# Kernel tuning notes

Measured on AMD Instinct MI355X. Metric: run time of the kernel, lower is better.

## Reference

```python
import jax, jax.numpy as jnp
import numpy as np

LN_EPS = 1e-5
NORM_EPS = 1e-12  # torch F.normalize default eps


def _layernorm(x, gamma, beta):
    mu = x.mean(axis=-1, keepdims=True)
    var = ((x - mu) ** 2).mean(axis=-1, keepdims=True)
    return (x - mu) * jax.lax.rsqrt(var + LN_EPS) * gamma + beta


def _l2norm(x, axis):
    n = jnp.sqrt((x ** 2).sum(axis=axis, keepdims=True))
    return x / jnp.maximum(n, NORM_EPS)


def setup_inputs() -> dict:
    key = jax.random.key(0)
    ks = jax.random.split(key, 4)
    B, N, D, E, S, H = 64, 256, 1024, 16, 16, 256
    x = jax.random.normal(ks[0], (B, N, D), dtype=jnp.float32)
    mu = jax.random.normal(ks[1], (D, E, S), dtype=jnp.float32) / np.sqrt(D)
    w1 = jax.random.normal(ks[2], (E, D, H), dtype=jnp.float32) * np.sqrt(2.0 / D)
    w2 = jax.random.normal(ks[3], (E, H, D), dtype=jnp.float32) * np.sqrt(2.0 / (H + D))
    return {
        'x': x,
        'ln_gamma': jnp.ones((D,), jnp.float32),
        'ln_beta': jnp.zeros((D,), jnp.float32),
        'mu': mu,
        'scale': jnp.ones((1,), jnp.float32),
        'w1': w1,
        'b1': jnp.zeros((E, H), jnp.float32),
        'w2': w2,
        'b2': jnp.zeros((E, D), jnp.float32),
    }


def reference(x, ln_gamma, ln_beta, mu, scale, w1, b1, w2, b2):
    B, N, D = x.shape
    _, E, S = mu.shape
    # LayerNorm then cosine-similarity logits (eval mode: no noise, no dropout)
    xn = _layernorm(x, ln_gamma, ln_beta)                      # [B,N,D]
    x_unit = _l2norm(xn, axis=-1)                              # [B,N,D]
    mu_unit = _l2norm(mu, axis=0)                              # [D,E,S]
    logits = jnp.einsum('bnd,des->bnes', x_unit * scale, mu_unit)  # [B,N,E,S]
    # dispatch: softmax over tokens n; combine: softmax over flattened slots (e,s)
    dispatch = jax.nn.softmax(logits, axis=1)                  # [B,N,E,S]
    combine = jax.nn.softmax(logits.reshape(B, N, E * S), axis=-1).reshape(B, N, E, S)
    # dispatch tokens to slots
    slot_in = jnp.einsum('bnd,bnes->besd', xn, dispatch)       # [B,E,S,D]
    # batched per-expert MLP (GELU exact, matches nn.GELU default)
    h = jax.nn.gelu(jnp.einsum('besd,edh->besh', slot_in, w1) + b1[None, :, None, :], approximate=False)
    slot_out = jnp.einsum('besh,ehd->besd', h, w2) + b2[None, :, None, :]
    # combine slots back to tokens
    out = jnp.einsum('besd,bnes->bnd', slot_out, combine)      # [B,N,D]
    return out
```

## Files before the change

### kernel.cpp

```cpp
#include <hip/hip_runtime.h>

#define DD 1024
#define NN 256
#define BB 64
#define EE 16
#define SS 16
#define HH 256
#define ES 256
#define BN 16384

typedef unsigned short u16;
typedef unsigned int u32;
typedef __attribute__((ext_vector_type(8))) short bf16x8;
typedef __attribute__((ext_vector_type(4))) float f32x4;

#define MFMA(a, b, c) __builtin_amdgcn_mfma_f32_16x16x32_bf16(a, b, c, 0, 0, 0)

__device__ __forceinline__ u16 f2b(float f) {
  union { float f; u32 i; } c; c.f = f;
  u32 i = c.i;
  u32 r = (i + 0x7FFFu + ((i >> 16) & 1u)) >> 16;
  return (u16)r;
}

__device__ __forceinline__ float bredsum(float v, float* red) {
  #pragma unroll
  for (int o = 32; o > 0; o >>= 1) v += __shfl_down(v, o, 64);
  __syncthreads();
  if ((threadIdx.x & 63) == 0) red[threadIdx.x >> 6] = v;
  __syncthreads();
  return red[0] + red[1] + red[2] + red[3];
}

__global__ __launch_bounds__(256) void k_stats(
    const float* __restrict__ x, const float* __restrict__ gamma,
    const float* __restrict__ beta, const float* __restrict__ scale,
    float* __restrict__ mean_, float* __restrict__ rstd_,
    float* __restrict__ fct_) {
  __shared__ float red[4];
  int bn = blockIdx.x, t = threadIdx.x;
  float4 u = ((const float4*)(x + (size_t)bn * DD))[t];
  float s = u.x + u.y + u.z + u.w;
  float ss = u.x * u.x + u.y * u.y + u.z * u.z + u.w * u.w;
  s = bredsum(s, red);
  ss = bredsum(ss, red);
  float mean = s * (1.0f / DD);
  float var = ss * (1.0f / DD) - mean * mean;
  float rstd = rsqrtf(var + 1e-5f);
  float4 g = ((const float4*)gamma)[t];
  float4 be = ((const float4*)beta)[t];
  float x0 = (u.x - mean) * rstd * g.x + be.x;
  float x1 = (u.y - mean) * rstd * g.y + be.y;
  float x2 = (u.z - mean) * rstd * g.z + be.z;
  float x3 = (u.w - mean) * rstd * g.w + be.w;
  float s2 = x0 * x0 + x1 * x1 + x2 * x2 + x3 * x3;
  s2 = bredsum(s2, red);
  float f = scale[0] / fmaxf(sqrtf(s2), 1e-12f);
  if (t == 0) { mean_[bn] = mean; rstd_[bn] = rstd; fct_[bn] = f; }
}

__global__ __launch_bounds__(256) void k_rmun(
    const float* __restrict__ mu, const float* __restrict__ gamma,
    const float* __restrict__ beta, float* __restrict__ rmun,
    float* __restrict__ c3, float* __restrict__ c4) {
  __shared__ float red[4];
  int es = blockIdx.x, t = threadIdx.x;
  float ss = 0.f, s3 = 0.f, s4 = 0.f;
  #pragma unroll
  for (int j = 0; j < 4; j++) {
    int d = t + j * 256;
    float v = mu[(size_t)d * ES + es];
    ss += v * v;
    s3 += gamma[d] * v;
    s4 += beta[d] * v;
  }
  ss = bredsum(ss, red);
  s3 = bredsum(s3, red);
  s4 = bredsum(s4, red);
  if (t == 0) {
    float r = 1.0f / fmaxf(sqrtf(ss), 1e-12f);
    rmun[es] = r;
    c3[es] = s3 * r;
    c4[es] = s4 * r;
  }
}

__global__ __launch_bounds__(256) void k_mut(
    const float* __restrict__ mu, const float* __restrict__ gamma,
    const float* __restrict__ rmun, u16* __restrict__ muT) {
  __shared__ u16 L[256 * 70];
  int t = threadIdx.x;
  int d0 = blockIdx.x * 64;
  float rm = rmun[t];
  for (int i = 0; i < 64; i++) {
    int d = d0 + i;
    float gv = gamma[d];
    L[t * 70 + i] = f2b(mu[(size_t)d * ES + t] * rm * gv);
  }
  __syncthreads();
  u32 buf[32];
  #pragma unroll
  for (int k2 = 0; k2 < 32; k2++)
    buf[k2] = *(const u32*)&L[t * 70 + k2 * 2];
  u16* dst = muT + (size_t)t * DD + d0;
  #pragma unroll
  for (int k4 = 0; k4 < 8; k4++) {
    uint4 o;
    o.x = buf[k4 * 4]; o.y = buf[k4 * 4 + 1];
    o.z = buf[k4 * 4 + 2]; o.w = buf[k4 * 4 + 3];
    *(uint4*)(dst + k4 * 8) = o;
  }
}

__global__ __launch_bounds__(256) void k_xt(
    const float* __restrict__ x, u16* __restrict__ xT) {
  __shared__ u16 L[256 * 70];
  int t = threadIdx.x;
  int bn0 = blockIdx.x * 64;
  for (int cch = 0; cch < 4; cch++) {
    __syncthreads();
    for (int r = 0; r < 64; r++)
      L[t * 70 + r] = f2b(x[(size_t)(bn0 + r) * DD + cch * 256 + t]);
    __syncthreads();
    u32 buf[32];
    #pragma unroll
    for (int k2 = 0; k2 < 32; k2++)
      buf[k2] = *(const u32*)&L[t * 70 + k2 * 2];
    u16* dst = xT + (size_t)(cch * 256 + t) * BN + bn0;
    #pragma unroll
    for (int k4 = 0; k4 < 8; k4++) {
      uint4 o;
      o.x = buf[k4 * 4]; o.y = buf[k4 * 4 + 1];
      o.z = buf[k4 * 4 + 2]; o.w = buf[k4 * 4 + 3];
      *(uint4*)(dst + k4 * 8) = o;
    }
  }
}

__global__ __launch_bounds__(256) void k_tr(
    const float* __restrict__ src, u16* __restrict__ dst, int R, int C) {
  __shared__ u16 T[64 * 70];
  int t = threadIdx.x;
  int e = blockIdx.y;
  int tR = R >> 6;
  int r0 = (blockIdx.x % tR) * 64;
  int c0 = (blockIdx.x / tR) * 64;
  #pragma unroll
  for (int i = 0; i < 16; i++) {
    int r = r0 + i * 4 + (t >> 6);
    int c = t & 63;
    T[c * 70 + i * 4 + (t >> 6)] = f2b(src[((size_t)e * R + r) * C + c0 + c]);
  }
  __syncthreads();
  int cl = t >> 2, rsg = (t & 3) * 16;
  u32 buf[8];
  #pragma unroll
  for (int k2 = 0; k2 < 8; k2++)
    buf[k2] = *(const u32*)&T[cl * 70 + rsg + k2 * 2];
  u16* dp = dst + ((size_t)e * C + c0 + cl) * R + r0 + rsg;
  uint4 o0, o1;
  o0.x = buf[0]; o0.y = buf[1]; o0.z = buf[2]; o0.w = buf[3];
  o1.x = buf[4]; o1.y = buf[5]; o1.z = buf[6]; o1.w = buf[7];
  *(uint4*)dp = o0;
  *(uint4*)(dp + 8) = o1;
}

__global__ __launch_bounds__(256) void k_logits_mfma(
    const float* __restrict__ x, const u16* __restrict__ muT,
    const float* __restrict__ mean_, const float* __restrict__ rstd_,
    const float* __restrict__ fct_, const float* __restrict__ c3,
    const float* __restrict__ c4, float* __restrict__ logitsT) {
  __shared__ u16 xb[64 * 136];
  int t = threadIdx.x;
  int lane = t & 63, w = t >> 6, q = lane >> 4, m16 = lane & 15;
  int bn0 = blockIdx.x * 64;
  int es0 = w * 64;
  f32x4 z = {0.f, 0.f, 0.f, 0.f};
  f32x4 acc[4][4];
  #pragma unroll
  for (int mt = 0; mt < 4; mt++)
    #pragma unroll
    for (int nt = 0; nt < 4; nt++) acc[mt][nt] = z;
  int sr = t >> 5, cc = (t & 31) * 4;
  for (int kb = 0; kb < 8; kb++) {
    __syncthreads();
    #pragma unroll
    for (int it = 0; it < 8; it++) {
      int row = sr + it * 8;
      float4 v = *(const float4*)(x + (size_t)(bn0 + row) * DD + kb * 128 + cc);
      uint2 pk;
      pk.x = (u32)f2b(v.x) | ((u32)f2b(v.y) << 16);
      pk.y = (u32)f2b(v.z) | ((u32)f2b(v.w) << 16);
      *(uint2*)&xb[row * 136 + cc] = pk;
    }
    __syncthreads();
    #pragma unroll
    for (int ks = 0; ks < 4; ks++) {
      int k = ks * 32 + q * 8;
      bf16x8 a[4];
      #pragma unroll
      for (int mt = 0; mt < 4; mt++)
        a[mt] = *(const bf16x8*)(muT + (size_t)(es0 + mt * 16 + m16) * DD +
                                 kb * 128 + k);
      #pragma unroll
      for (int nt = 0; nt < 4; nt++) {
        bf16x8 bb = *(const bf16x8*)&xb[(nt * 16 + m16) * 136 + k];
        #pragma unroll
        for (int mt = 0; mt < 4; mt++)
          acc[mt][nt] = MFMA(a[mt], bb, acc[mt][nt]);
      }
    }
  }
  #pragma unroll
  for (int nt = 0; nt < 4; nt++) {
    int bn = bn0 + nt * 16 + m16;
    float fv = fct_[bn], rv = rstd_[bn], mv = mean_[bn];
    #pragma unroll
    for (int mt = 0; mt < 4; mt++)
      #pragma unroll
      for (int i = 0; i < 4; i++) {
        int es = es0 + mt * 16 + q * 4 + i;
        float val = fv * (rv * acc[mt][nt][i] - rv * mv * c3[es] + c4[es]);
        logitsT[(size_t)es * BN + bn] = val;
      }
  }
}

__global__ __launch_bounds__(256) void k_disp(
    const float* __restrict__ logitsT, const float* __restrict__ mean_,
    const float* __restrict__ rstd_, u16* __restrict__ dispW,
    float* __restrict__ c1g) {
  int t = threadIdx.x;
  int e = blockIdx.x, b = blockIdx.y;
  int s = t >> 4, c = t & 15;
  const float* lrow = logitsT + (size_t)(e * 16 + s) * BN + b * 256 + c * 16;
  float lv[16];
  #pragma unroll
  for (int i2 = 0; i2 < 4; i2++) {
    float4 f = *(const float4*)(lrow + i2 * 4);
    lv[i2 * 4 + 0] = f.x; lv[i2 * 4 + 1] = f.y;
    lv[i2 * 4 + 2] = f.z; lv[i2 * 4 + 3] = f.w;
  }
  float mx = -1e30f;
  #pragma unroll
  for (int i = 0; i < 16; i++) mx = fmaxf(mx, lv[i]);
  #pragma unroll
  for (int o = 1; o < 16; o <<= 1) mx = fmaxf(mx, __shfl_xor(mx, o, 64));
  float sum = 0.f;
  #pragma unroll
  for (int i = 0; i < 16; i++) { lv[i] = __expf(lv[i] - mx); sum += lv[i]; }
  #pragma unroll
  for (int o = 1; o < 16; o <<= 1) sum += __shfl_xor(sum, o, 64);
  float inv = 1.0f / sum;
  float c1p = 0.f;
  u16 wp[16];
  #pragma unroll
  for (int i = 0; i < 16; i++) {
    int n = c * 16 + i;
    float wv = lv[i] * inv * rstd_[b * 256 + n];
    c1p += wv * mean_[b * 256 + n];
    wp[i] = f2b(wv);
  }
  #pragma unroll
  for (int o = 1; o < 16; o <<= 1) c1p += __shfl_xor(c1p, o, 64);
  if (c == 0) c1g[(b << 8) + e * 16 + s] = c1p;
  u16* drow = dispW + ((size_t)(b * 256 + e * 16 + s)) * 256 + c * 16;
  #pragma unroll
  for (int i2 = 0; i2 < 4; i2++) {
    uint2 pk;
    pk.x = (u32)wp[i2 * 4] | ((u32)wp[i2 * 4 + 1] << 16);
    pk.y = (u32)wp[i2 * 4 + 2] | ((u32)wp[i2 * 4 + 3] << 16);
    *(uint2*)(drow + i2 * 4) = pk;
  }
}

__global__ __launch_bounds__(256) void k_slotin(
    const u16* __restrict__ xT, const u16* __restrict__ dispW,
    const float* __restrict__ c1g, const float* __restrict__ gamma,
    const float* __restrict__ beta, u16* __restrict__ SI) {
  __shared__ u16 xb[128 * 264];
  int t = threadIdx.x;
  int lane = t & 63, w = t >> 6, q = lane >> 4, m16 = lane & 15;
  int d0 = blockIdx.x * 128, b = blockIdx.y;
  #pragma unroll
  for (int it = 0; it < 16; it++) {
    int c = it * 256 + t;
    int row = c >> 5, off = (c & 31) * 8;
    uint4 v = *(const uint4*)(xT + (size_t)(d0 + row) * BN + b * 256 + off);
    *(uint4*)&xb[row * 264 + off] = v;
  }
  __syncthreads();
  f32x4 z = {0.f, 0.f, 0.f, 0.f};
  f32x4 acc[4][8];
  #pragma unroll
  for (int mt = 0; mt < 4; mt++)
    #pragma unroll
    for (int nt = 0; nt < 8; nt++) acc[mt][nt] = z;
  int es0 = w * 64;
  for (int ks = 0; ks < 8; ks++) {
    int k = ks * 32 + q * 8;
    bf16x8 a[4];
    #pragma unroll
    for (int mt = 0; mt < 4; mt++)
      a[mt] = *(const bf16x8*)(dispW +
               ((size_t)(b * 256 + es0 + mt * 16 + m16)) * 256 + k);
    #pragma unroll
    for (int nt = 0; nt < 8; nt++) {
      bf16x8 bb = *(const bf16x8*)&xb[(nt * 16 + m16) * 264 + k];
      #pragma unroll
      for (int mt = 0; mt < 4; mt++) acc[mt][nt] = MFMA(a[mt], bb, acc[mt][nt]);
    }
  }
  float gv[8], bev[8];
  #pragma unroll
  for (int nt = 0; nt < 8; nt++) {
    int d = d0 + nt * 16 + m16;
    gv[nt] = gamma[d]; bev[nt] = beta[d];
  }
  #pragma unroll
  for (int mt = 0; mt < 4; mt++) {
    float c1[4];
    #pragma unroll
    for (int i = 0; i < 4; i++)
      c1[i] = c1g[(b << 8) + es0 + mt * 16 + q * 4 + i];
    #pragma unroll
    for (int nt = 0; nt < 8; nt++)
      #pragma unroll
      for (int i = 0; i < 4; i++)
        SI[((size_t)(w * 4 + mt) * 1024 + b * 16 + q * 4 + i) * DD + d0 +
           nt * 16 + m16] = f2b(gv[nt] * (acc[mt][nt][i] - c1[i]) + bev[nt]);
  }
}

__global__ __launch_bounds__(256) void k_mlp1(
    const u16* __restrict__ SI, const u16* __restrict__ w1T,
    const float* __restrict__ b1, u16* __restrict__ H) {
  __shared__ u16 At[64 * 72];
  __shared__ u16 Bt[64 * 72];
  int t = threadIdx.x;
  int lane = t & 63, w = t >> 6, q = lane >> 4, m16 = lane & 15;
  int nt0 = blockIdx.x * 64;
  int mt0 = blockIdx.y * 64;
  int e = blockIdx.z;
  int wm = (w & 1) * 32, wn = (w >> 1) * 32;
  f32x4 z = {0.f, 0.f, 0.f, 0.f};
  f32x4 acc[2][2];
  #pragma unroll
  for (int mt = 0; mt < 2; mt++)
    #pragma unroll
    for (int nt = 0; nt < 2; nt++) acc[mt][nt] = z;
  const u16* Ab = SI + ((size_t)e * 1024 + mt0) * DD;
  const u16* Bb = w1T + ((size_t)e * HH + nt0) * DD;
  int row = t >> 2, off = (t & 3) * 16;
  uint4 pa0, pa1, pb0, pb1;
  pa0 = *(const uint4*)(Ab + (size_t)row * DD + off);
  pa1 = *(const uint4*)(Ab + (size_t)row * DD + off + 8);
  pb0 = *(const uint4*)(Bb + (size_t)row * DD + off);
  pb1 = *(const uint4*)(Bb + (size_t)row * DD + off + 8);
  for (int kb = 0; kb < 16; kb++) {
    *(uint4*)&At[row * 72 + off] = pa0;
    *(uint4*)&At[row * 72 + off + 8] = pa1;
    *(uint4*)&Bt[row * 72 + off] = pb0;
    *(uint4*)&Bt[row * 72 + off + 8] = pb1;
    __syncthreads();
    if (kb < 15) {
      int k0 = (kb + 1) * 64;
      pa0 = *(const uint4*)(Ab + (size_t)row * DD + k0 + off);
      pa1 = *(const uint4*)(Ab + (size_t)row * DD + k0 + off + 8);
      pb0 = *(const uint4*)(Bb + (size_t)row * DD + k0 + off);
      pb1 = *(const uint4*)(Bb + (size_t)row * DD + k0 + off + 8);
    }
    #pragma unroll
    for (int kk = 0; kk < 2; kk++) {
      int k = kk * 32 + q * 8;
      bf16x8 a[2], bb[2];
      #pragma unroll
      for (int mt = 0; mt < 2; mt++)
        a[mt] = *(const bf16x8*)&At[(wm + mt * 16 + m16) * 72 + k];
      #pragma unroll
      for (int nt = 0; nt < 2; nt++)
        bb[nt] = *(const bf16x8*)&Bt[(wn + nt * 16 + m16) * 72 + k];
      #pragma unroll
      for (int mt = 0; mt < 2; mt++)
        #pragma unroll
        for (int nt = 0; nt < 2; nt++)
          acc[mt][nt] = MFMA(a[mt], bb[nt], acc[mt][nt]);
    }
    __syncthreads();
  }
  #pragma unroll
  for (int nt = 0; nt < 2; nt++) {
    int h = nt0 + wn + nt * 16 + m16;
    float b1v = b1[e * HH + h];
    #pragma unroll
    for (int mt = 0; mt < 2; mt++)
      #pragma unroll
      for (int i = 0; i < 4; i++) {
        float zz = acc[mt][nt][i] + b1v;
        int bs = mt0 + wm + mt * 16 + q * 4 + i;
        H[((size_t)e * 1024 + bs) * HH + h] =
            f2b(0.5f * zz * (1.0f + erff(zz * 0.70710678118654752f)));
      }
  }
}

__global__ __launch_bounds__(256) void k_mlp2(
    const u16* __restrict__ H, const u16* __restrict__ w2T,
    const float* __restrict__ b2, u16* __restrict__ SO) {
  __shared__ u16 At[128 * 72];
  __shared__ u16 Bt[128 * 72];
  int t = threadIdx.x;
  int lane = t & 63, w = t >> 6, q = lane >> 4, m16 = lane & 15;
  int nt0 = blockIdx.x * 128;
  int mt0 = blockIdx.y * 128;
  int e = blockIdx.z;
  int wm = (w & 1) * 64, wn = (w >> 1) * 64;
  f32x4 z = {0.f, 0.f, 0.f, 0.f};
  f32x4 acc[4][4];
  #pragma unroll
  for (int mt = 0; mt < 4; mt++)
    #pragma unroll
    for (int nt = 0; nt < 4; nt++) acc[mt][nt] = z;
  const u16* Ab = H + ((size_t)e * 1024 + mt0) * HH;
  const u16* Bb = w2T + ((size_t)e * DD + nt0) * HH;
  for (int kb = 0; kb < 4; kb++) {
    __syncthreads();
    #pragma unroll
    for (int it = 0; it < 4; it++) {
      int c = it * 256 + t;
      int row = c >> 3, off = (c & 7) * 8;
      *(uint4*)&At[row * 72 + off] =
          *(const uint4*)(Ab + (size_t)row * HH + kb * 64 + off);
      *(uint4*)&Bt[row * 72 + off] =
          *(const uint4*)(Bb + (size_t)row * HH + kb * 64 + off);
    }
    __syncthreads();
    #pragma unroll
    for (int kk = 0; kk < 2; kk++) {
      int k = kk * 32 + q * 8;
      bf16x8 a[4], bb[4];
      #pragma unroll
      for (int mt = 0; mt < 4; mt++)
        a[mt] = *(const bf16x8*)&At[(wm + mt * 16 + m16) * 72 + k];
      #pragma unroll
      for (int nt = 0; nt < 4; nt++)
        bb[nt] = *(const bf16x8*)&Bt[(wn + nt * 16 + m16) * 72 + k];
      #pragma unroll
      for (int mt = 0; mt < 4; mt++)
        #pragma unroll
        for (int nt = 0; nt < 4; nt++)
          acc[mt][nt] = MFMA(a[mt], bb[nt], acc[mt][nt]);
    }
  }
  #pragma unroll
  for (int nt = 0; nt < 4; nt++) {
    int d = nt0 + wn + nt * 16 + m16;
    float b2v = b2[e * DD + d];
    #pragma unroll
    for (int mt = 0; mt < 4; mt++)
      #pragma unroll
      for (int i = 0; i < 4; i++) {
        int bs = mt0 + wm + mt * 16 + q * 4 + i;
        SO[((size_t)e * 1024 + bs) * DD + d] = f2b(acc[mt][nt][i] + b2v);
      }
  }
}

__global__ __launch_bounds__(256) void k_out_mfma(
    const u16* __restrict__ slot_out, const float* __restrict__ logitsT,
    float* __restrict__ out) {
  __shared__ u16 comb[32 * 264];
  __shared__ u16 sot[64 * 264];
  __shared__ float red[8][32];
  int t = threadIdx.x;
  int lane = t & 63, w = t >> 6, q = lane >> 4, m16 = lane & 15;
  int id = blockIdx.x;
  int b = (id & 7) * 8 + ((id >> 3) & 7);
  int dc = id >> 6;
  {
    int es2 = (t & 127) * 2, dh = t >> 7;
    const u16* s0 = slot_out +
        ((size_t)((es2 >> 4) * 1024 + b * 16 + (es2 & 15))) * DD +
        dc * 64 + dh * 32;
    const u16* s1 = s0 + DD;
    #pragma unroll
    for (int k2 = 0; k2 < 8; k2++) {
      ushort4 r0 = *(const ushort4*)(s0 + k2 * 4);
      ushort4 r1 = *(const ushort4*)(s1 + k2 * 4);
      int dl = dh * 32 + k2 * 4;
      *(u32*)&sot[(dl + 0) * 264 + es2] = (u32)r0.x | ((u32)r1.x << 16);
      *(u32*)&sot[(dl + 1) * 264 + es2] = (u32)r0.y | ((u32)r1.y << 16);
      *(u32*)&sot[(dl + 2) * 264 + es2] = (u32)r0.z | ((u32)r1.z << 16);
      *(u32*)&sot[(dl + 3) * 264 + es2] = (u32)r0.w | ((u32)r1.w << 16);
    }
  }
  for (int nch = 0; nch < 8; nch++) {
    int n0 = nch * 32;
    __syncthreads();
    {
      int j = t & 31, ch = t >> 5;
      float lv[32];
      const float* base = logitsT + (size_t)(ch * 32) * BN + b * 256 + n0 + j;
      #pragma unroll
      for (int i = 0; i < 32; i++) lv[i] = base[(size_t)i * BN];
      float mx = -1e30f;
      #pragma unroll
      for (int i = 0; i < 32; i++) mx = fmaxf(mx, lv[i]);
      red[ch][j] = mx;
      __syncthreads();
      mx = red[0][j];
      #pragma unroll
      for (int k = 1; k < 8; k++) mx = fmaxf(mx, red[k][j]);
      __syncthreads();
      float sum = 0.f;
      #pragma unroll
      for (int i = 0; i < 32; i++) { lv[i] = __expf(lv[i] - mx); sum += lv[i]; }
      red[ch][j] = sum;
      __syncthreads();
      sum = 0.f;
      #pragma unroll
      for (int k = 0; k < 8; k++) sum += red[k][j];
      float inv = 1.0f / sum;
      #pragma unroll
      for (int i2 = 0; i2 < 8; i2++) {
        uint2 pk;
        pk.x = (u32)f2b(lv[i2 * 4] * inv) | ((u32)f2b(lv[i2 * 4 + 1] * inv) << 16);
        pk.y = (u32)f2b(lv[i2 * 4 + 2] * inv) | ((u32)f2b(lv[i2 * 4 + 3] * inv) << 16);
        *(uint2*)&comb[j * 264 + ch * 32 + i2 * 4] = pk;
      }
    }
    __syncthreads();
    f32x4 aA = {0.f, 0.f, 0.f, 0.f}, aB = {0.f, 0.f, 0.f, 0.f};
    #pragma unroll
    for (int ks = 0; ks < 8; ks++) {
      bf16x8 bb = *(const bf16x8*)&sot[(w * 16 + m16) * 264 + ks * 32 + q * 8];
      bf16x8 a0 = *(const bf16x8*)&comb[m16 * 264 + ks * 32 + q * 8];
      bf16x8 a1 = *(const bf16x8*)&comb[(16 + m16) * 264 + ks * 32 + q * 8];
      aA = MFMA(a0, bb, aA);
      aB = MFMA(a1, bb, aB);
    }
    int d = dc * 64 + w * 16 + m16;
    #pragma unroll
    for (int i = 0; i < 4; i++) {
      out[((size_t)b * NN + n0 + q * 4 + i) * DD + d] = aA[i];
      out[((size_t)b * NN + n0 + 16 + q * 4 + i) * DD + d] = aB[i];
    }
  }
}

extern "C" void kernel_launch(void* const* d_in, const int* in_sizes, int n_in,
                              void* d_out, int out_size, void* d_ws, size_t ws_size,
                              hipStream_t stream) {
  const float* x     = (const float*)d_in[0];
  const float* gamma = (const float*)d_in[1];
  const float* beta  = (const float*)d_in[2];
  const float* mu    = (const float*)d_in[3];
  const float* scale = (const float*)d_in[4];
  const float* w1    = (const float*)d_in[5];
  const float* b1    = (const float*)d_in[6];
  const float* w2    = (const float*)d_in[7];
  const float* b2    = (const float*)d_in[8];
  float* out = (float*)d_out;

  const size_t WS_NEED = 50531328;
  if (ws_size < WS_NEED) return;
  char* ws = (char*)d_ws;
  u16*   sislot  = (u16*)(ws);
  float* logitsT = (float*)(ws + 33554432);
  float* mean_   = (float*)(ws + 50331648);
  float* rstd_   = (float*)(ws + 50397184);
  float* fct_    = (float*)(ws + 50462720);
  float* rmun    = (float*)(ws + 50528256);
  float* c3      = (float*)(ws + 50529280);
  float* c4      = (float*)(ws + 50530304);

  char* sc = (char*)d_out;
  u16* xT    = (u16*)(sc);
  u16* w1T   = (u16*)(sc + 33554432);
  u16* w2T   = (u16*)(sc + 41943040);
  u16* dispW = (u16*)(sc + 50331648);
  u16* muT   = (u16*)(sc + 58720256);
  float* c1g = (float*)(sc + 59244544);
  u16* Hbuf  = (u16*)(sc + 58720256);

  k_stats<<<BN, 256, 0, stream>>>(x, gamma, beta, scale, mean_, rstd_, fct_);
  k_rmun<<<ES, 256, 0, stream>>>(mu, gamma, beta, rmun, c3, c4);
  k_mut<<<16, 256, 0, stream>>>(mu, gamma, rmun, muT);
  k_xt<<<BN / 64, 256, 0, stream>>>(x, xT);
  k_tr<<<dim3(64, EE), 256, 0, stream>>>(w1, w1T, DD, HH);
  k_tr<<<dim3(64, EE), 256, 0, stream>>>(w2, w2T, HH, DD);
  k_logits_mfma<<<BN / 64, 256, 0, stream>>>(x, muT, mean_, rstd_, fct_,
                                             c3, c4, logitsT);
  k_disp<<<dim3(EE, BB), 256, 0, stream>>>(logitsT, mean_, rstd_, dispW, c1g);
  k_slotin<<<dim3(8, BB), 256, 0, stream>>>(xT, dispW, c1g, gamma, beta, sislot);
  k_mlp1<<<dim3(4, 16, EE), 256, 0, stream>>>(sislot, w1T, b1, Hbuf);
  k_mlp2<<<dim3(8, 8, EE), 256, 0, stream>>>(Hbuf, w2T, b2, sislot);
  k_out_mfma<<<dim3(1024), 256, 0, stream>>>(sislot, logitsT, out);
}
```

Baseline: 375.5 us.

## Precompute combine softmax in separate kernel and prefetch x tiles in logits GEMM

Adds a k_comb kernel that turns logitsT in place into combine-softmax probabilities right after the dispatch pass. k_out_mfma then reads those probabilities directly instead of recomputing the softmax eight times per batch with several block barriers. The logits kernel also register-prefetches the next fp32 x tile while the MFMAs run. The new softmax skips max subtraction, which relies on cosine-bounded logits (|logit| ≤ scale) to stay safe from overflow, and it adds a launch plus an extra read-write pass over logitsT.

```diff
diff --git a/kernel.cpp b/kernel.cpp
--- a/kernel.cpp
+++ b/kernel.cpp
@@ -182,18 +182,27 @@
     #pragma unroll
     for (int nt = 0; nt < 4; nt++) acc[mt][nt] = z;
   int sr = t >> 5, cc = (t & 31) * 4;
+  float4 pf[8];
+  #pragma unroll
+  for (int it = 0; it < 8; it++)
+    pf[it] = *(const float4*)(x + (size_t)(bn0 + sr + it * 8) * DD + cc);
   for (int kb = 0; kb < 8; kb++) {
     __syncthreads();
     #pragma unroll
     for (int it = 0; it < 8; it++) {
       int row = sr + it * 8;
-      float4 v = *(const float4*)(x + (size_t)(bn0 + row) * DD + kb * 128 + cc);
       uint2 pk;
-      pk.x = (u32)f2b(v.x) | ((u32)f2b(v.y) << 16);
-      pk.y = (u32)f2b(v.z) | ((u32)f2b(v.w) << 16);
+      pk.x = (u32)f2b(pf[it].x) | ((u32)f2b(pf[it].y) << 16);
+      pk.y = (u32)f2b(pf[it].z) | ((u32)f2b(pf[it].w) << 16);
       *(uint2*)&xb[row * 136 + cc] = pk;
     }
     __syncthreads();
+    if (kb < 7) {
+      #pragma unroll
+      for (int it = 0; it < 8; it++)
+        pf[it] = *(const float4*)(x + (size_t)(bn0 + sr + it * 8) * DD +
+                                  (kb + 1) * 128 + cc);
+    }
     #pragma unroll
     for (int ks = 0; ks < 4; ks++) {
       int k = ks * 32 + q * 8;
@@ -272,6 +281,28 @@
     pk.y = (u32)wp[i2 * 4 + 2] | ((u32)wp[i2 * 4 + 3] << 16);
     *(uint2*)(drow + i2 * 4) = pk;
   }
+}
+
+__global__ __launch_bounds__(256) void k_comb(float* __restrict__ logitsT) {
+  __shared__ float red[4][64];
+  int t = threadIdx.x;
+  int l = t & 63, g = t >> 6;
+  int bn = blockIdx.y * 256 + blockIdx.x * 64 + l;
+  float* base = logitsT + (size_t)(g * 64) * BN + bn;
+  float ev[64];
+  float sum = 0.f;
+  #pragma unroll
+  for (int i = 0; i < 64; i++) {
+    float e = __expf(base[(size_t)i * BN]);
+    ev[i] = e;
+    sum += e;
+  }
+  red[g][l] = sum;
+  __syncthreads();
+  float inv = 1.0f / (red[0][l] + red[1][l] + red[2][l] + red[3][l]);
+  #pragma unroll
+  for (int i = 0; i < 64; i++)
+    base[(size_t)i * BN] = ev[i] * inv;
 }
 
 __global__ __launch_bounds__(256) void k_slotin(
@@ -471,7 +502,6 @@
     float* __restrict__ out) {
   __shared__ u16 comb[32 * 264];
   __shared__ u16 sot[64 * 264];
-  __shared__ float red[8][32];
   int t = threadIdx.x;
   int lane = t & 63, w = t >> 6, q = lane >> 4, m16 = lane & 15;
   int id = blockIdx.x;
@@ -499,33 +529,15 @@
     __syncthreads();
     {
       int j = t & 31, ch = t >> 5;
+      const float* base = logitsT + (size_t)(ch * 32) * BN + b * 256 + n0 + j;
       float lv[32];
-      const float* base = logitsT + (size_t)(ch * 32) * BN + b * 256 + n0 + j;
       #pragma unroll
       for (int i = 0; i < 32; i++) lv[i] = base[(size_t)i * BN];
-      float mx = -1e30f;
-      #pragma unroll
-      for (int i = 0; i < 32; i++) mx = fmaxf(mx, lv[i]);
-      red[ch][j] = mx;
-      __syncthreads();
-      mx = red[0][j];
-      #pragma unroll
-      for (int k = 1; k < 8; k++) mx = fmaxf(mx, red[k][j]);
-      __syncthreads();
-      float sum = 0.f;
-      #pragma unroll
-      for (int i = 0; i < 32; i++) { lv[i] = __expf(lv[i] - mx); sum += lv[i]; }
-      red[ch][j] = sum;
-      __syncthreads();
-      sum = 0.f;
-      #pragma unroll
-      for (int k = 0; k < 8; k++) sum += red[k][j];
-      float inv = 1.0f / sum;
       #pragma unroll
       for (int i2 = 0; i2 < 8; i2++) {
         uint2 pk;
-        pk.x = (u32)f2b(lv[i2 * 4] * inv) | ((u32)f2b(lv[i2 * 4 + 1] * inv) << 16);
-        pk.y = (u32)f2b(lv[i2 * 4 + 2] * inv) | ((u32)f2b(lv[i2 * 4 + 3] * inv) << 16);
+        pk.x = (u32)f2b(lv[i2 * 4]) | ((u32)f2b(lv[i2 * 4 + 1]) << 16);
+        pk.y = (u32)f2b(lv[i2 * 4 + 2]) | ((u32)f2b(lv[i2 * 4 + 3]) << 16);
         *(uint2*)&comb[j * 264 + ch * 32 + i2 * 4] = pk;
       }
     }
@@ -592,6 +604,7 @@
   k_logits_mfma<<<BN / 64, 256, 0, stream>>>(x, muT, mean_, rstd_, fct_,
                                              c3, c4, logitsT);
   k_disp<<<dim3(EE, BB), 256, 0, stream>>>(logitsT, mean_, rstd_, dispW, c1g);
+  k_comb<<<dim3(4, BB), 256, 0, stream>>>(logitsT);
   k_slotin<<<dim3(8, BB), 256, 0, stream>>>(xT, dispW, c1g, gamma, beta, sislot);
   k_mlp1<<<dim3(4, 16, EE), 256, 0, stream>>>(sislot, w1T, b1, Hbuf);
   k_mlp2<<<dim3(8, 8, EE), 256, 0, stream>>>(Hbuf, w2T, b2, sislot);
```

Result: no change. 379.4 us (+1.0%).
